# Optimization experiments

Hardware: AMD Instinct MI355X
Metric: run time of the kernel (lower is better)

## Reference

```python
import jax, jax.numpy as jnp
import numpy as np

SEQ_LEN = 180
LATENT = 128
HIDDEN = 256
BATCH = 8192


def setup_inputs() -> dict:
    key = jax.random.key(0)
    ks = jax.random.split(key, 9)
    s = 1.0 / np.sqrt(HIDDEN)
    return {
        "z": jax.random.normal(ks[0], (BATCH, LATENT), jnp.float32),
        "fc_w": jax.random.normal(ks[1], (HIDDEN, LATENT), jnp.float32) * (1.0 / np.sqrt(LATENT)),
        "fc_b": jax.random.normal(ks[2], (HIDDEN,), jnp.float32) * 0.1,
        "w_ih": jax.random.normal(ks[3], (3 * HIDDEN, 2), jnp.float32) * s,
        "b_ih": jax.random.normal(ks[4], (3 * HIDDEN,), jnp.float32) * s,
        "w_hh": jax.random.normal(ks[5], (3 * HIDDEN, HIDDEN), jnp.float32) * s,
        "b_hh": jax.random.normal(ks[6], (3 * HIDDEN,), jnp.float32) * s,
        "out_w": jax.random.normal(ks[7], (2, HIDDEN), jnp.float32) * s,
        "out_b": jax.random.normal(ks[8], (2,), jnp.float32) * 0.1,
    }


def reference(z, fc_w, fc_b, w_ih, b_ih, w_hh, b_hh, out_w, out_b):
    # h0 = tanh(fc(z))  -> [B, H]
    h0 = jnp.tanh(z @ fc_w.T + fc_b)
    B = z.shape[0]
    # GRU input is all-zeros, so input-hidden gates are a constant bias: [B, 3H]
    gi = jnp.zeros((B, 2), z.dtype) @ w_ih.T + b_ih
    gi_r, gi_z, gi_n = jnp.split(gi, 3, axis=-1)

    def step(h, _):
        gh = h @ w_hh.T + b_hh                 # [B, 3H]
        gh_r, gh_z, gh_n = jnp.split(gh, 3, axis=-1)
        r = jax.nn.sigmoid(gi_r + gh_r)
        zg = jax.nn.sigmoid(gi_z + gh_z)
        n = jnp.tanh(gi_n + r * gh_n)
        h_new = (1.0 - zg) * n + zg * h
        return h_new, h_new

    _, hs = jax.lax.scan(step, h0, None, length=SEQ_LEN)  # [T, B, H]
    hs = jnp.swapaxes(hs, 0, 1)                            # [B, T, H]
    return hs @ out_w.T + out_b                            # [B, T, 2]
```

## Files before the change

kernel.cpp:

```cpp
#include <hip/hip_runtime.h>
#include <hip/hip_bf16.h>

#define T_SEQ  180
#define LATENT 128
#define HIDDEN 256

typedef __attribute__((ext_vector_type(8))) short  short8;
typedef __attribute__((ext_vector_type(4))) float  floatx4;
typedef __attribute__((ext_vector_type(4))) int    intx4;
typedef __attribute__((ext_vector_type(2))) float  float2v;

#define LOG2E 1.4426950408889634f

#define WQ_OFF    0
#define FCW_OFF   196608
#define SCW_OFF   262144
#define OUTW_OFF  265216
#define SWOUT_OFF 269312

#define H8_STRIDE  272
#define H8B_OFF    8704
#define OBUF_OFF   17408
#define OBUF_HALF  256
#define SMEM_BYTES 19456

__device__ __forceinline__ unsigned short f2bf(float f) {
    unsigned int u = __float_as_uint(f);
    u += 0x7fffu + ((u >> 16) & 1u);
    return (unsigned short)(u >> 16);
}

__global__ void pack_scales(const float* __restrict__ whh, float* __restrict__ scales) {
    int wid  = blockIdx.x * 4 + (threadIdx.x >> 6);
    int lane = threadIdx.x & 63;
    const float* src = whh + (size_t)wid * 256 + lane * 4;
    float m = 0.0f;
#pragma unroll
    for (int j = 0; j < 4; ++j) m = fmaxf(m, fabsf(src[j]));
#pragma unroll
    for (int d = 1; d < 64; d <<= 1) m = fmaxf(m, __shfl_xor(m, d, 64));
    if (lane == 0) scales[wid] = m;
}

__global__ void pack_whh_i8(const float* __restrict__ whh, const float* __restrict__ scales,
                            signed char* __restrict__ dst) {
    int tid  = blockIdx.x * blockDim.x + threadIdx.x;
    int lane = tid & 63;
    int frag = tid >> 6;
    int kc   = frag & 3;
    int sub  = (frag >> 2) % 6;
    int w    = frag / 24;
    int g = sub >> 1, cs = sub & 1;
    int col  = w * 32 + cs * 16 + (lane & 15);
    int jout = g * 256 + col;
    int k0   = kc * 64 + ((lane >> 4) << 4);
    const float* src = whh + (size_t)jout * 256 + k0;
    float inv = 127.0f / scales[jout];
    signed char q[16];
#pragma unroll
    for (int j = 0; j < 16; ++j) {
        float v = __builtin_rintf(src[j] * inv);
        v = fminf(fmaxf(v, -127.0f), 127.0f);
        q[j] = (signed char)(int)v;
    }
    *(intx4*)(dst + (size_t)frag * 1024 + lane * 16) = *(intx4*)q;
}

__global__ void pack_fcw(const float* __restrict__ fcw, unsigned short* __restrict__ dst) {
    int tid  = blockIdx.x * blockDim.x + threadIdx.x;
    int lane = tid & 63;
    int frag = tid >> 6;
    int kc   = frag & 3;
    int cs   = (frag >> 2) & 1;
    int w    = frag >> 3;
    int col  = w * 32 + cs * 16 + (lane & 15);
    int k0   = kc * 32 + ((lane >> 4) << 3);
    const float* src = fcw + col * 128 + k0;
    unsigned int u[4];
#pragma unroll
    for (int j = 0; j < 4; ++j)
        u[j] = (unsigned int)f2bf(src[2 * j]) | ((unsigned int)f2bf(src[2 * j + 1]) << 16);
    *(uint4*)(dst + frag * 512 + lane * 8) = make_uint4(u[0], u[1], u[2], u[3]);
}

__global__ void pack_outw_i8(const float* __restrict__ out_w,
                             signed char* __restrict__ dst, float* __restrict__ swout) {
    __shared__ float sw[2];
    int tid = threadIdx.x;
    if (tid < 128) {
        int o = tid >> 6, lane = tid & 63;
        const float* src = out_w + o * 256 + lane * 4;
        float m = 0.0f;
#pragma unroll
        for (int j = 0; j < 4; ++j) m = fmaxf(m, fabsf(src[j]));
#pragma unroll
        for (int d = 1; d < 64; d <<= 1) m = fmaxf(m, __shfl_xor(m, d, 64));
        if (lane == 0) { sw[o] = m; swout[o] = m; }
    }
    __syncthreads();
    int sl = tid >> 6, lane = tid & 63;
    int n  = lane & 15;
    int k0 = sl * 64 + ((lane >> 4) << 4);
    signed char q[16];
#pragma unroll
    for (int j = 0; j < 16; ++j) {
        float v = 0.0f;
        if (n < 2) {
            v = __builtin_rintf(out_w[n * 256 + k0 + j] * (127.0f / sw[n]));
            v = fminf(fmaxf(v, -127.0f), 127.0f);
        }
        q[j] = (signed char)(int)v;
    }
    *(intx4*)(dst + sl * 1024 + lane * 16) = *(intx4*)q;
}

__global__ __launch_bounds__(1024, 4) void gru_main(
    const float* __restrict__ z,
    const float* __restrict__ fc_b,
    const float* __restrict__ b_ih,
    const float* __restrict__ b_hh,
    const float* __restrict__ out_b,
    const unsigned char* __restrict__ ws,
    float* __restrict__ out)
{
    extern __shared__ unsigned char smem[];
    signed char* h8a   = (signed char*)smem;
    signed char* h8b   = (signed char*)(smem + H8B_OFF);
    int*         obufI = (int*)(smem + OBUF_OFF);

    const int tid  = threadIdx.x;
    const int lane = tid & 63;
    const int wv   = tid >> 6;
    const int cg   = wv;
    const int l15  = lane & 15;
    const int qd   = lane >> 4;
    const int rh   = (wv >> 2) & 1;
    const int sl   = wv & 3;
    const int rb   = blockIdx.x * 32;
    const int wsw  = (l15 >> 2) & 3;

    const intx4 zero4 = (intx4){0, 0, 0, 0};

    intx4 wq[12];
#pragma unroll
    for (int g = 0; g < 3; ++g)
#pragma unroll
        for (int kc = 0; kc < 4; ++kc)
            wq[g * 4 + kc] = *(const intx4*)(ws + WQ_OFF
                + (size_t)((((cg >> 1) * 6 + g * 2 + (cg & 1)) * 4 + kc)) * 1024 + lane * 16);

    intx4 bproj = *(const intx4*)(ws + OUTW_OFF + sl * 1024 + lane * 16);
    const float* swout = (const float*)(ws + SWOUT_OFF);
    float pscF = swout[lane & 1] * (1.0f / 16129.0f);

    const float* scales = (const float*)(ws + SCW_OFF);
    float fcbE2;
    float2v nscqr2, ncbr2, nscqz2, ncbz2, scqn2, bhn2, bin2;
    {
        int col = cg * 16 + l15;
        float ncbrE  = -(b_ih[col]       + b_hh[col])       * LOG2E;
        float ncbzE  = -(b_ih[256 + col] + b_hh[256 + col]) * LOG2E;
        float binE2  = b_ih[512 + col] * (2.0f * LOG2E);
        float bhnE2  = b_hh[512 + col] * (2.0f * LOG2E);
        fcbE2  = fc_b[col] * (2.0f * LOG2E);
        float nscqrE = -scales[col]       * (LOG2E / 16129.0f);
        float nscqzE = -scales[256 + col] * (LOG2E / 16129.0f);
        float scqnE2 = scales[512 + col] * (2.0f * LOG2E / 16129.0f);
        nscqr2 = (float2v){nscqrE, nscqrE};  ncbr2 = (float2v){ncbrE, ncbrE};
        nscqz2 = (float2v){nscqzE, nscqzE};  ncbz2 = (float2v){ncbzE, ncbzE};
        scqn2  = (float2v){scqnE2, scqnE2};  bhn2  = (float2v){bhnE2, bhnE2};
        bin2   = (float2v){binE2, binE2};
    }
    const float2v m254 = (float2v){-254.0f, -254.0f};
    const float2v p127 = (float2v){127.0f, 127.0f};
    float ob = out_b[lane & 1];

    const int rdOff = l15 * H8_STRIDE + (qd ^ wsw) * 16;
    const int pjOff = (rh * 16 + l15) * H8_STRIDE + sl * 64 + (qd ^ wsw) * 16;
    const int wrOff = (qd * 4) * H8_STRIDE + ((cg ^ qd) & 15) * 16 + l15;

    const int rlW = ((wv - 8) * 4 + (lane >> 1)) & 31;
    const int o8  = lane & 1;
    const int fbase = (rlW >> 4) * 128 + (rlW & 15) * 2 + o8;
    float* opW8 = out + (size_t)(rb + rlW) * (T_SEQ * 2) + o8;

    floatx4 a0f[2];
#pragma unroll
    for (int rt = 0; rt < 2; ++rt) a0f[rt] = (floatx4){0.f, 0.f, 0.f, 0.f};
#pragma unroll
    for (int kc = 0; kc < 4; ++kc) {
        short8 bfr = *(const short8*)(ws + FCW_OFF + (size_t)(cg * 4 + kc) * 1024 + lane * 16);
#pragma unroll
        for (int rt = 0; rt < 2; ++rt) {
            const float* zp = z + (size_t)(rb + rt * 16 + l15) * LATENT + kc * 32 + qd * 8;
            short8 afr;
#pragma unroll
            for (int j = 0; j < 8; ++j) afr[j] = (short)f2bf(zp[j]);
            a0f[rt] = __builtin_amdgcn_mfma_f32_16x16x32_bf16(afr, bfr, a0f[rt], 0, 0, 0);
        }
    }

    float2v hm2[2][2];
#pragma unroll
    for (int rt = 0; rt < 2; ++rt)
#pragma unroll
        for (int r = 0; r < 4; ++r) {
            float u = __builtin_amdgcn_rcpf(1.0f + __builtin_amdgcn_exp2f(
                          __builtin_fmaf(a0f[rt][r], 2.0f * LOG2E, fcbE2)));
            float h = __builtin_fmaf(-254.0f, u, 127.0f);
            hm2[rt][r >> 1][r & 1] = h;
            h8a[wrOff + rt * (16 * H8_STRIDE) + r * H8_STRIDE] =
                (signed char)__float_as_uint(h + 12582912.0f);
        }
    __syncthreads();

    intx4 acc0[3], acc1[3];

#define HUPD_PAIR(ACC, RT, P, WP)                                                 \
    {                                                                             \
        float2v arv, azv, anv;                                                    \
        arv[0] = (float)(ACC)[0][2*(P)];   arv[1] = (float)(ACC)[0][2*(P)+1];     \
        azv[0] = (float)(ACC)[1][2*(P)];   azv[1] = (float)(ACC)[1][2*(P)+1];     \
        anv[0] = (float)(ACC)[2][2*(P)];   anv[1] = (float)(ACC)[2][2*(P)+1];     \
        float2v yr = __builtin_elementwise_fma(arv, nscqr2, ncbr2);               \
        float2v yz = __builtin_elementwise_fma(azv, nscqz2, ncbz2);               \
        float2v Ar, Az;                                                           \
        Ar[0] = __builtin_amdgcn_exp2f(yr[0]); Ar[1] = __builtin_amdgcn_exp2f(yr[1]); \
        Az[0] = __builtin_amdgcn_exp2f(yz[0]); Az[1] = __builtin_amdgcn_exp2f(yz[1]); \
        float2v dr = Ar + 1.0f, dz = Az + 1.0f;                                   \
        float2v pr = dr * dz;                                                     \
        float2v q_;                                                               \
        q_[0] = __builtin_amdgcn_rcpf(pr[0]); q_[1] = __builtin_amdgcn_rcpf(pr[1]); \
        float2v gr = q_ * dz, gz = q_ * dr;                                       \
        float2v xn2 = __builtin_elementwise_fma(anv, scqn2, bhn2);                \
        float2v tt  = __builtin_elementwise_fma(gr, xn2, bin2);                   \
        float2v Ee, uu;                                                           \
        Ee[0] = __builtin_amdgcn_exp2f(tt[0]); Ee[1] = __builtin_amdgcn_exp2f(tt[1]); \
        Ee = Ee + 1.0f;                                                           \
        uu[0] = __builtin_amdgcn_rcpf(Ee[0]); uu[1] = __builtin_amdgcn_rcpf(Ee[1]); \
        float2v gn = __builtin_elementwise_fma(m254, uu, p127);                   \
        float2v hv = hm2[RT][P];                                                  \
        float2v hn = __builtin_elementwise_fma(gz, hv - gn, gn);                  \
        hm2[RT][P] = hn;                                                          \
        float2v hb = hn + 12582912.0f;                                            \
        (WP)[(2*(P))   * H8_STRIDE] = (signed char)__float_as_uint(hb[0]);        \
        (WP)[(2*(P)+1) * H8_STRIDE] = (signed char)__float_as_uint(hb[1]);        \
    }

#define GRU_STEP(H8P, H8N, OBR, OBW, DO_STASH, DO_FLUSH)                         \
    {                                                                            \
        const signed char* rp0 = (H8P) + rdOff;                                  \
        const signed char* rp1 = rp0 + 16 * H8_STRIDE;                           \
        signed char*       wp0 = (H8N) + wrOff;                                  \
        signed char*       wp1 = wp0 + 16 * H8_STRIDE;                           \
        intx4 pj;                                                                \
        if (DO_STASH && wv < 8) {                                                \
            intx4 a8p = *(const intx4*)((H8P) + pjOff);                          \
            pj = __builtin_amdgcn_mfma_i32_16x16x64_i8(a8p, bproj, zero4, 0, 0, 0); \
        }                                                                        \
        if (DO_FLUSH && wv >= 8 && lane < 8) {                                   \
            int s_ = (OBR)[fbase] + (OBR)[fbase + 32]                            \
                   + (OBR)[fbase + 64] + (OBR)[fbase + 96];                      \
            *opW8 = __builtin_fmaf((float)s_, pscF, ob);                         \
            opW8 += 2;                                                           \
        }                                                                        \
        intx4 a8 = *(const intx4*)(rp0);                                         \
        acc0[0] = __builtin_amdgcn_mfma_i32_16x16x64_i8(a8, wq[0], zero4,   0, 0, 0); \
        acc0[1] = __builtin_amdgcn_mfma_i32_16x16x64_i8(a8, wq[4], zero4,   0, 0, 0); \
        acc0[2] = __builtin_amdgcn_mfma_i32_16x16x64_i8(a8, wq[8], zero4,   0, 0, 0); \
        a8 = *(const intx4*)(rp1);                                               \
        acc1[0] = __builtin_amdgcn_mfma_i32_16x16x64_i8(a8, wq[0], zero4,   0, 0, 0); \
        acc1[1] = __builtin_amdgcn_mfma_i32_16x16x64_i8(a8, wq[4], zero4,   0, 0, 0); \
        acc1[2] = __builtin_amdgcn_mfma_i32_16x16x64_i8(a8, wq[8], zero4,   0, 0, 0); \
        a8 = *(const intx4*)(rp0 + 64);                                          \
        acc0[0] = __builtin_amdgcn_mfma_i32_16x16x64_i8(a8, wq[1], acc0[0], 0, 0, 0); \
        acc0[1] = __builtin_amdgcn_mfma_i32_16x16x64_i8(a8, wq[5], acc0[1], 0, 0, 0); \
        acc0[2] = __builtin_amdgcn_mfma_i32_16x16x64_i8(a8, wq[9], acc0[2], 0, 0, 0); \
        a8 = *(const intx4*)(rp1 + 64);                                          \
        acc1[0] = __builtin_amdgcn_mfma_i32_16x16x64_i8(a8, wq[1], acc1[0], 0, 0, 0); \
        acc1[1] = __builtin_amdgcn_mfma_i32_16x16x64_i8(a8, wq[5], acc1[1], 0, 0, 0); \
        acc1[2] = __builtin_amdgcn_mfma_i32_16x16x64_i8(a8, wq[9], acc1[2], 0, 0, 0); \
        a8 = *(const intx4*)(rp0 + 128);                                         \
        acc0[0] = __builtin_amdgcn_mfma_i32_16x16x64_i8(a8, wq[2], acc0[0], 0, 0, 0); \
        acc0[1] = __builtin_amdgcn_mfma_i32_16x16x64_i8(a8, wq[6], acc0[1], 0, 0, 0); \
        acc0[2] = __builtin_amdgcn_mfma_i32_16x16x64_i8(a8, wq[10], acc0[2], 0, 0, 0); \
        a8 = *(const intx4*)(rp1 + 128);                                         \
        acc1[0] = __builtin_amdgcn_mfma_i32_16x16x64_i8(a8, wq[2], acc1[0], 0, 0, 0); \
        acc1[1] = __builtin_amdgcn_mfma_i32_16x16x64_i8(a8, wq[6], acc1[1], 0, 0, 0); \
        acc1[2] = __builtin_amdgcn_mfma_i32_16x16x64_i8(a8, wq[10], acc1[2], 0, 0, 0); \
        a8 = *(const intx4*)(rp0 + 192);                                         \
        acc0[0] = __builtin_amdgcn_mfma_i32_16x16x64_i8(a8, wq[3], acc0[0], 0, 0, 0); \
        acc0[1] = __builtin_amdgcn_mfma_i32_16x16x64_i8(a8, wq[7], acc0[1], 0, 0, 0); \
        acc0[2] = __builtin_amdgcn_mfma_i32_16x16x64_i8(a8, wq[11], acc0[2], 0, 0, 0); \
        a8 = *(const intx4*)(rp1 + 192);                                         \
        acc1[0] = __builtin_amdgcn_mfma_i32_16x16x64_i8(a8, wq[3], acc1[0], 0, 0, 0); \
        acc1[1] = __builtin_amdgcn_mfma_i32_16x16x64_i8(a8, wq[7], acc1[1], 0, 0, 0); \
        acc1[2] = __builtin_amdgcn_mfma_i32_16x16x64_i8(a8, wq[11], acc1[2], 0, 0, 0); \
        HUPD_PAIR(acc0, 0, 0, wp0)                                               \
        HUPD_PAIR(acc0, 0, 1, wp0)                                               \
        HUPD_PAIR(acc1, 1, 0, wp1)                                               \
        HUPD_PAIR(acc1, 1, 1, wp1)                                               \
        if (DO_STASH && wv < 8 && l15 < 2) {                                     \
            _Pragma("unroll")                                                    \
            for (int r = 0; r < 4; ++r)                                          \
                (OBW)[(rh * 4 + sl) * 32 + (qd * 4 + r) * 2 + l15] = pj[r];      \
        }                                                                        \
        __syncthreads();                                                         \
    }

    int* ob0 = obufI;
    int* ob1 = obufI + OBUF_HALF;

    GRU_STEP(h8a, h8b, ob1, ob0, 0, 0)
    GRU_STEP(h8b, h8a, ob0, ob1, 1, 0)

#pragma unroll 1
    for (int t2 = 0; t2 < 89; ++t2) {
        GRU_STEP(h8a, h8b, ob1, ob0, 1, 1)
        GRU_STEP(h8b, h8a, ob0, ob1, 1, 1)
    }

    if (wv < 8) {
        intx4 a8p = *(const intx4*)(h8a + pjOff);
        intx4 pj = __builtin_amdgcn_mfma_i32_16x16x64_i8(a8p, bproj, zero4, 0, 0, 0);
        if (l15 < 2)
#pragma unroll
            for (int r = 0; r < 4; ++r)
                ob0[(rh * 4 + sl) * 32 + (qd * 4 + r) * 2 + l15] = pj[r];
    }
    if (wv >= 8 && lane < 8) {
        int s_ = ob1[fbase] + ob1[fbase + 32] + ob1[fbase + 64] + ob1[fbase + 96];
        *opW8 = __builtin_fmaf((float)s_, pscF, ob);
        opW8 += 2;
    }
    __syncthreads();
    if (wv >= 8 && lane < 8) {
        int s_ = ob0[fbase] + ob0[fbase + 32] + ob0[fbase + 64] + ob0[fbase + 96];
        *opW8 = __builtin_fmaf((float)s_, pscF, ob);
    }
#undef GRU_STEP
#undef HUPD_PAIR
}

extern "C" void kernel_launch(void* const* d_in, const int* in_sizes, int n_in,
                              void* d_out, int out_size, void* d_ws, size_t ws_size,
                              hipStream_t stream) {
    const float* z     = (const float*)d_in[0];
    const float* fc_w  = (const float*)d_in[1];
    const float* fc_b  = (const float*)d_in[2];
    const float* b_ih  = (const float*)d_in[4];
    const float* w_hh  = (const float*)d_in[5];
    const float* b_hh  = (const float*)d_in[6];
    const float* out_w = (const float*)d_in[7];
    const float* out_b = (const float*)d_in[8];
    float* out = (float*)d_out;
    unsigned char* ws = (unsigned char*)d_ws;

    hipFuncSetAttribute((const void*)gru_main,
                        hipFuncAttributeMaxDynamicSharedMemorySize, SMEM_BYTES);

    pack_scales<<<192, 256, 0, stream>>>(w_hh, (float*)(ws + SCW_OFF));
    pack_whh_i8<<<48, 256, 0, stream>>>(w_hh, (const float*)(ws + SCW_OFF),
                                        (signed char*)(ws + WQ_OFF));
    pack_fcw<<<16, 256, 0, stream>>>(fc_w, (unsigned short*)(ws + FCW_OFF));
    pack_outw_i8<<<1, 256, 0, stream>>>(out_w, (signed char*)(ws + OUTW_OFF),
                                        (float*)(ws + SWOUT_OFF));
    gru_main<<<256, 1024, SMEM_BYTES, stream>>>(z, fc_b, b_ih, b_hh, out_b, ws, out);
}
```

Before: 474.4 us.

## Stagger MFMA and gate-update phases across waves with priority hints

```diff
diff --git a/kernel.cpp b/kernel.cpp
--- a/kernel.cpp
+++ b/kernel.cpp
@@ -138,6 +138,8 @@
     const int sl   = wv & 3;
     const int rb   = blockIdx.x * 32;
     const int wsw  = (l15 >> 2) & 3;
+
+    const int rtSel = (wv ^ (wv >> 2)) & 1;
 
     const intx4 zero4 = (intx4){0, 0, 0, 0};
 
@@ -179,6 +181,9 @@
     const int pjOff = (rh * 16 + l15) * H8_STRIDE + sl * 64 + (qd ^ wsw) * 16;
     const int wrOff = (qd * 4) * H8_STRIDE + ((cg ^ qd) & 15) * 16 + l15;
 
+    const int tA = rtSel * (16 * H8_STRIDE);
+    const int tB = (1 - rtSel) * (16 * H8_STRIDE);
+
     const int rlW = ((wv - 8) * 4 + (lane >> 1)) & 31;
     const int o8  = lane & 1;
     const int fbase = (rlW >> 4) * 128 + (rlW & 15) * 2 + o8;
@@ -201,20 +206,32 @@
     }
 
     float2v hm2[2][2];
-#pragma unroll
-    for (int rt = 0; rt < 2; ++rt)
-#pragma unroll
-        for (int r = 0; r < 4; ++r) {
-            float u = __builtin_amdgcn_rcpf(1.0f + __builtin_amdgcn_exp2f(
-                          __builtin_fmaf(a0f[rt][r], 2.0f * LOG2E, fcbE2)));
-            float h = __builtin_fmaf(-254.0f, u, 127.0f);
-            hm2[rt][r >> 1][r & 1] = h;
-            h8a[wrOff + rt * (16 * H8_STRIDE) + r * H8_STRIDE] =
-                (signed char)__float_as_uint(h + 12582912.0f);
-        }
+    {
+        float t0[4], t1[4];
+#pragma unroll
+        for (int rt = 0; rt < 2; ++rt)
+#pragma unroll
+            for (int r = 0; r < 4; ++r) {
+                float u = __builtin_amdgcn_rcpf(1.0f + __builtin_amdgcn_exp2f(
+                              __builtin_fmaf(a0f[rt][r], 2.0f * LOG2E, fcbE2)));
+                float h = __builtin_fmaf(-254.0f, u, 127.0f);
+                if (rt == 0) t0[r] = h; else t1[r] = h;
+                h8a[wrOff + rt * (16 * H8_STRIDE) + r * H8_STRIDE] =
+                    (signed char)__float_as_uint(h + 12582912.0f);
+            }
+#pragma unroll
+        for (int P = 0; P < 2; ++P)
+#pragma unroll
+            for (int j = 0; j < 2; ++j) {
+                hm2[0][P][j] = rtSel ? t1[2 * P + j] : t0[2 * P + j];
+                hm2[1][P][j] = rtSel ? t0[2 * P + j] : t1[2 * P + j];
+            }
+    }
     __syncthreads();
 
     intx4 acc0[3], acc1[3];
+
+#define MFI8(A, B, C) __builtin_amdgcn_mfma_i32_16x16x64_i8((A), (B), (C), 0, 0, 0)
 
 #define HUPD_PAIR(ACC, RT, P, WP)                                                 \
     {                                                                             \
@@ -247,65 +264,88 @@
         (WP)[(2*(P)+1) * H8_STRIDE] = (signed char)__float_as_uint(hb[1]);        \
     }
 
-#define GRU_STEP(H8P, H8N, OBR, OBW, DO_STASH, DO_FLUSH)                         \
-    {                                                                            \
-        const signed char* rp0 = (H8P) + rdOff;                                  \
-        const signed char* rp1 = rp0 + 16 * H8_STRIDE;                           \
-        signed char*       wp0 = (H8N) + wrOff;                                  \
-        signed char*       wp1 = wp0 + 16 * H8_STRIDE;                           \
-        intx4 pj;                                                                \
-        if (DO_STASH && wv < 8) {                                                \
-            intx4 a8p = *(const intx4*)((H8P) + pjOff);                          \
-            pj = __builtin_amdgcn_mfma_i32_16x16x64_i8(a8p, bproj, zero4, 0, 0, 0); \
-        }                                                                        \
-        if (DO_FLUSH && wv >= 8 && lane < 8) {                                   \
-            int s_ = (OBR)[fbase] + (OBR)[fbase + 32]                            \
-                   + (OBR)[fbase + 64] + (OBR)[fbase + 96];                      \
-            *opW8 = __builtin_fmaf((float)s_, pscF, ob);                         \
-            opW8 += 2;                                                           \
-        }                                                                        \
-        intx4 a8 = *(const intx4*)(rp0);                                         \
-        acc0[0] = __builtin_amdgcn_mfma_i32_16x16x64_i8(a8, wq[0], zero4,   0, 0, 0); \
-        acc0[1] = __builtin_amdgcn_mfma_i32_16x16x64_i8(a8, wq[4], zero4,   0, 0, 0); \
-        acc0[2] = __builtin_amdgcn_mfma_i32_16x16x64_i8(a8, wq[8], zero4,   0, 0, 0); \
-        a8 = *(const intx4*)(rp1);                                               \
-        acc1[0] = __builtin_amdgcn_mfma_i32_16x16x64_i8(a8, wq[0], zero4,   0, 0, 0); \
-        acc1[1] = __builtin_amdgcn_mfma_i32_16x16x64_i8(a8, wq[4], zero4,   0, 0, 0); \
-        acc1[2] = __builtin_amdgcn_mfma_i32_16x16x64_i8(a8, wq[8], zero4,   0, 0, 0); \
-        a8 = *(const intx4*)(rp0 + 64);                                          \
-        acc0[0] = __builtin_amdgcn_mfma_i32_16x16x64_i8(a8, wq[1], acc0[0], 0, 0, 0); \
-        acc0[1] = __builtin_amdgcn_mfma_i32_16x16x64_i8(a8, wq[5], acc0[1], 0, 0, 0); \
-        acc0[2] = __builtin_amdgcn_mfma_i32_16x16x64_i8(a8, wq[9], acc0[2], 0, 0, 0); \
-        a8 = *(const intx4*)(rp1 + 64);                                          \
-        acc1[0] = __builtin_amdgcn_mfma_i32_16x16x64_i8(a8, wq[1], acc1[0], 0, 0, 0); \
-        acc1[1] = __builtin_amdgcn_mfma_i32_16x16x64_i8(a8, wq[5], acc1[1], 0, 0, 0); \
-        acc1[2] = __builtin_amdgcn_mfma_i32_16x16x64_i8(a8, wq[9], acc1[2], 0, 0, 0); \
-        a8 = *(const intx4*)(rp0 + 128);                                         \
-        acc0[0] = __builtin_amdgcn_mfma_i32_16x16x64_i8(a8, wq[2], acc0[0], 0, 0, 0); \
-        acc0[1] = __builtin_amdgcn_mfma_i32_16x16x64_i8(a8, wq[6], acc0[1], 0, 0, 0); \
-        acc0[2] = __builtin_amdgcn_mfma_i32_16x16x64_i8(a8, wq[10], acc0[2], 0, 0, 0); \
-        a8 = *(const intx4*)(rp1 + 128);                                         \
-        acc1[0] = __builtin_amdgcn_mfma_i32_16x16x64_i8(a8, wq[2], acc1[0], 0, 0, 0); \
-        acc1[1] = __builtin_amdgcn_mfma_i32_16x16x64_i8(a8, wq[6], acc1[1], 0, 0, 0); \
-        acc1[2] = __builtin_amdgcn_mfma_i32_16x16x64_i8(a8, wq[10], acc1[2], 0, 0, 0); \
-        a8 = *(const intx4*)(rp0 + 192);                                         \
-        acc0[0] = __builtin_amdgcn_mfma_i32_16x16x64_i8(a8, wq[3], acc0[0], 0, 0, 0); \
-        acc0[1] = __builtin_amdgcn_mfma_i32_16x16x64_i8(a8, wq[7], acc0[1], 0, 0, 0); \
-        acc0[2] = __builtin_amdgcn_mfma_i32_16x16x64_i8(a8, wq[11], acc0[2], 0, 0, 0); \
-        a8 = *(const intx4*)(rp1 + 192);                                         \
-        acc1[0] = __builtin_amdgcn_mfma_i32_16x16x64_i8(a8, wq[3], acc1[0], 0, 0, 0); \
-        acc1[1] = __builtin_amdgcn_mfma_i32_16x16x64_i8(a8, wq[7], acc1[1], 0, 0, 0); \
-        acc1[2] = __builtin_amdgcn_mfma_i32_16x16x64_i8(a8, wq[11], acc1[2], 0, 0, 0); \
-        HUPD_PAIR(acc0, 0, 0, wp0)                                               \
-        HUPD_PAIR(acc0, 0, 1, wp0)                                               \
-        HUPD_PAIR(acc1, 1, 0, wp1)                                               \
-        HUPD_PAIR(acc1, 1, 1, wp1)                                               \
-        if (DO_STASH && wv < 8 && l15 < 2) {                                     \
-            _Pragma("unroll")                                                    \
-            for (int r = 0; r < 4; ++r)                                          \
-                (OBW)[(rh * 4 + sl) * 32 + (qd * 4 + r) * 2 + l15] = pj[r];      \
-        }                                                                        \
-        __syncthreads();                                                         \
+#define CLUST_A(RPA) {                                                            \
+        intx4 a8 = *(const intx4*)(RPA);                                          \
+        acc0[0] = MFI8(a8, wq[0], zero4);                                         \
+        acc0[1] = MFI8(a8, wq[4], zero4);                                         \
+        acc0[2] = MFI8(a8, wq[8], zero4);                                         \
+        a8 = *(const intx4*)((RPA) + 64);                                         \
+        acc0[0] = MFI8(a8, wq[1], acc0[0]);                                       \
+        acc0[1] = MFI8(a8, wq[5], acc0[1]);                                       \
+        acc0[2] = MFI8(a8, wq[9], acc0[2]);                                       \
+        a8 = *(const intx4*)((RPA) + 128);                                        \
+        acc0[0] = MFI8(a8, wq[2], acc0[0]);                                       \
+        acc0[1] = MFI8(a8, wq[6], acc0[1]);                                       \
+        acc0[2] = MFI8(a8, wq[10], acc0[2]);                                      \
+        a8 = *(const intx4*)((RPA) + 192);                                        \
+        acc0[0] = MFI8(a8, wq[3], acc0[0]);                                       \
+        acc0[1] = MFI8(a8, wq[7], acc0[1]);                                       \
+        acc0[2] = MFI8(a8, wq[11], acc0[2]);                                      \
+    }
+#define CLUST_B01(RPB) {                                                          \
+        intx4 a8 = *(const intx4*)(RPB);                                          \
+        acc1[0] = MFI8(a8, wq[0], zero4);                                         \
+        acc1[1] = MFI8(a8, wq[4], zero4);                                         \
+        acc1[2] = MFI8(a8, wq[8], zero4);                                         \
+        a8 = *(const intx4*)((RPB) + 64);                                         \
+        acc1[0] = MFI8(a8, wq[1], acc1[0]);                                       \
+        acc1[1] = MFI8(a8, wq[5], acc1[1]);                                       \
+        acc1[2] = MFI8(a8, wq[9], acc1[2]);                                       \
+    }
+#define CLUST_B23(RPB) {                                                          \
+        intx4 a8 = *(const intx4*)((RPB) + 128);                                  \
+        acc1[0] = MFI8(a8, wq[2], acc1[0]);                                       \
+        acc1[1] = MFI8(a8, wq[6], acc1[1]);                                       \
+        acc1[2] = MFI8(a8, wq[10], acc1[2]);                                      \
+        a8 = *(const intx4*)((RPB) + 192);                                        \
+        acc1[0] = MFI8(a8, wq[3], acc1[0]);                                       \
+        acc1[1] = MFI8(a8, wq[7], acc1[1]);                                       \
+        acc1[2] = MFI8(a8, wq[11], acc1[2]);                                      \
+    }
+#define FLUSH(OBR) {                                                              \
+        int s_ = (OBR)[fbase] + (OBR)[fbase + 32]                                 \
+               + (OBR)[fbase + 64] + (OBR)[fbase + 96];                           \
+        *opW8 = __builtin_fmaf((float)s_, pscF, ob);                              \
+        opW8 += 2;                                                                \
+    }
+#define STASH(OBW) {                                                              \
+        _Pragma("unroll")                                                         \
+        for (int r = 0; r < 4; ++r)                                               \
+            (OBW)[(rh * 4 + sl) * 32 + (qd * 4 + r) * 2 + l15] = pj[r];           \
+    }
+
+#define GRU_STEP(H8P, H8N, OBR, OBW, DO_STASH, DO_FLUSH)                          \
+    {                                                                             \
+        const signed char* rpA = (H8P) + rdOff + tA;                              \
+        const signed char* rpB = (H8P) + rdOff + tB;                              \
+        signed char*       wpA = (H8N) + wrOff + tA;                              \
+        signed char*       wpB = (H8N) + wrOff + tB;                              \
+        intx4 pj;                                                                 \
+        if (DO_STASH && wv < 8) {                                                 \
+            intx4 a8p = *(const intx4*)((H8P) + pjOff);                           \
+            pj = MFI8(a8p, bproj, zero4);                                         \
+        }                                                                         \
+        if (rtSel == 0) {                                                         \
+            __builtin_amdgcn_s_setprio(1);                                        \
+            CLUST_A(rpA) CLUST_B01(rpB) CLUST_B23(rpB)                            \
+            __builtin_amdgcn_s_setprio(0);                                        \
+            if (DO_FLUSH && wv >= 8 && lane < 8) { FLUSH(OBR) }                   \
+            HUPD_PAIR(acc0, 0, 0, wpA) HUPD_PAIR(acc0, 0, 1, wpA)                 \
+            HUPD_PAIR(acc1, 1, 0, wpB) HUPD_PAIR(acc1, 1, 1, wpB)                 \
+        } else {                                                                  \
+            __builtin_amdgcn_s_setprio(1);                                        \
+            CLUST_A(rpA) CLUST_B01(rpB)                                           \
+            __builtin_amdgcn_s_setprio(0);                                        \
+            HUPD_PAIR(acc0, 0, 0, wpA)                                            \
+            if (DO_FLUSH && wv >= 8 && lane < 8) { FLUSH(OBR) }                   \
+            HUPD_PAIR(acc0, 0, 1, wpA)                                            \
+            __builtin_amdgcn_s_setprio(1);                                        \
+            CLUST_B23(rpB)                                                        \
+            __builtin_amdgcn_s_setprio(0);                                        \
+            HUPD_PAIR(acc1, 1, 0, wpB) HUPD_PAIR(acc1, 1, 1, wpB)                 \
+        }                                                                         \
+        if (DO_STASH && wv < 8 && l15 < 2) { STASH(OBW) }                         \
+        __syncthreads();                                                          \
     }
 
     int* ob0 = obufI;
@@ -322,7 +362,7 @@
 
     if (wv < 8) {
         intx4 a8p = *(const intx4*)(h8a + pjOff);
-        intx4 pj = __builtin_amdgcn_mfma_i32_16x16x64_i8(a8p, bproj, zero4, 0, 0, 0);
+        intx4 pj = MFI8(a8p, bproj, zero4);
         if (l15 < 2)
 #pragma unroll
             for (int r = 0; r < 4; ++r)
@@ -339,7 +379,13 @@
         *opW8 = __builtin_fmaf((float)s_, pscF, ob);
     }
 #undef GRU_STEP
+#undef STASH
+#undef FLUSH
+#undef CLUST_B23
+#undef CLUST_B01
+#undef CLUST_A
 #undef HUPD_PAIR
+#undef MFI8
 }
 
 extern "C" void kernel_launch(void* const* d_in, const int* in_sizes, int n_in,
```

Measured after the change: 470.4 us. About the same (-0.8%).
